# Kernel optimization log

Hardware: AMD Instinct MI355X
Metric: run time of the kernel (lower is better)

## Reference

```python
import jax, jax.numpy as jnp
import numpy as np

B, T, D = 4, 2048, 2048
DI = int(D * 2.0)  # mlp_expansion = 2.0
RMS_EPS = 1e-6
LRU_EPS = 1e-6
INIT_SCALE = 0.02


def _rmsnorm(x, w):
    return x * jax.lax.rsqrt(jnp.mean(x * x, axis=-1, keepdims=True) + RMS_EPS) * w


def setup_inputs() -> dict:
    key = jax.random.key(0)
    ks = jax.random.split(key, 10)
    s = INIT_SCALE
    return {
        "x": jax.random.normal(ks[0], (B, T, D), dtype=jnp.float32),
        "state": jnp.zeros((B, D), dtype=jnp.float32),
        "w_norm1": jnp.ones((D,), dtype=jnp.float32),
        "W_in": jax.random.normal(ks[1], (D, D), dtype=jnp.float32) * s,
        "W_r": jax.random.normal(ks[2], (D, D), dtype=jnp.float32) * s,
        "b_r": jnp.zeros((D,), dtype=jnp.float32),
        "W_i": jax.random.normal(ks[3], (D, D), dtype=jnp.float32) * s,
        "b_i": jnp.zeros((D,), dtype=jnp.float32),
        "log_decay": jax.random.normal(ks[4], (D,), dtype=jnp.float32),
        "W_out": jax.random.normal(ks[5], (D, D), dtype=jnp.float32) * s,
        "w_norm2": jnp.ones((D,), dtype=jnp.float32),
        "W_gate": jax.random.normal(ks[6], (DI, D), dtype=jnp.float32) * s,
        "W_up": jax.random.normal(ks[7], (DI, D), dtype=jnp.float32) * s,
        "W_down": jax.random.normal(ks[8], (D, DI), dtype=jnp.float32) * s,
    }


def reference(x, state, w_norm1, W_in, W_r, b_r, W_i, b_i, log_decay,
              W_out, w_norm2, W_gate, W_up, W_down):
    # --- pre-norm + RG-LRU mixer ---
    n = _rmsnorm(x, w_norm1)                      # (B,T,D)
    r = jax.nn.sigmoid(n @ W_r.T + b_r)           # input gate
    g = jax.nn.sigmoid(n @ W_i.T + b_i)           # recurrent gate
    xp = n @ W_in.T                               # projected input
    alpha = jnp.clip(jax.nn.sigmoid(log_decay), LRU_EPS, 1.0 - LRU_EPS)  # (D,)
    scale = jnp.sqrt(jnp.clip(1.0 - alpha * alpha, 0.0, None))           # (D,)
    b_seq = scale * (r * xp)                      # (B,T,D)

    def step(h, b_t):                             # h_t = alpha*h + scale*(r_t*x_t)
        h = alpha * h + b_t
        return h, h

    h_final, hs = jax.lax.scan(step, state, jnp.swapaxes(b_seq, 0, 1))  # hs: (T,B,D)
    hs = jnp.swapaxes(hs, 0, 1)                   # (B,T,D)
    mixer_out = (hs * g) @ W_out.T
    x = x + mixer_out

    # --- SwiGLU FFN ---
    n2 = _rmsnorm(x, w_norm2)
    ffn = (jax.nn.silu(n2 @ W_gate.T) * (n2 @ W_up.T)) @ W_down.T
    return x + ffn, h_final
```

## Files before the change

### kernel.cpp

```cpp
#include <hip/hip_runtime.h>

#define BD 4
#define TD 2048
#define DD 2048
#define DID 4096
#define MD (BD*TD)
#define CHK 32
#define CHL (TD/CHK)

typedef float f32x4 __attribute__((ext_vector_type(4)));
typedef short s16x8 __attribute__((ext_vector_type(8)));
typedef unsigned short u16;
typedef unsigned short u16x4 __attribute__((ext_vector_type(4)));
typedef unsigned short u16x8 __attribute__((ext_vector_type(8)));

__device__ __forceinline__ float bf2f(u16 u) {
    union { unsigned int i; float f; } v; v.i = ((unsigned int)u) << 16; return v.f;
}
__device__ __forceinline__ u16 f2bf(float f) {
    union { float f; unsigned int i; } v; v.f = f;
    unsigned int r = v.i + 0x7fffu + ((v.i >> 16) & 1u);
    return (u16)(r >> 16);
}
__device__ __forceinline__ float sigm(float x) { return 1.f / (1.f + __expf(-x)); }

__device__ __forceinline__ void mfma16(f32x4& acc, s16x8 a, s16x8 b) {
    asm("v_mfma_f32_16x16x32_bf16 %0, %1, %2, %0" : "+v"(acc) : "v"(a), "v"(b));
}

__device__ __forceinline__ void gload16(const u16* g, u16* l) {
    __builtin_amdgcn_global_load_lds((__attribute__((address_space(1))) void*)(g),
                                     (__attribute__((address_space(3))) void*)(l),
                                     16, 0, 0);
}

__global__ __launch_bounds__(256)
void cvt_all(const float4* __restrict__ sr, const float4* __restrict__ sin_,
             const float4* __restrict__ si, const float4* __restrict__ sout,
             const float4* __restrict__ sg, const float4* __restrict__ su,
             const float4* __restrict__ sd, u16x4* __restrict__ dst, int n4) {
    const int SEG  = DD * DD / 4;
    const int ROWQ = DD / 4;
    int i = blockIdx.x * blockDim.x + threadIdx.x;
    int stride = gridDim.x * blockDim.x;
    for (; i < n4; i += stride) {
        const float4* s; int off; size_t di;
        if (i < 2 * SEG) {
            int which = i / SEG;
            int jj = i - which * SEG;
            int g = jj / ROWQ, cq = jj - g * ROWQ;
            int nb = g >> 6, ii = g & 63;
            int dr = which == 0 ? nb * 128 + (ii < 32 ? ii : ii + 32)
                                : nb * 128 + (ii < 32 ? ii + 32 : ii + 64);
            s = which ? sin_ : sr; off = jj;
            di = (size_t)dr * ROWQ + cq;
        } else if (i < 3 * SEG) {
            s = si; off = i - 2 * SEG; di = i;
        } else if (i < 4 * SEG) {
            s = sout; off = i - 3 * SEG; di = i;
        } else if (i < 8 * SEG) {
            int j = i - 4 * SEG;
            int which = j / (2 * SEG);
            int jj = j - which * 2 * SEG;
            int g = jj / ROWQ, cq = jj - g * ROWQ;
            int nb = g >> 6, ii = g & 63;
            int dr = which == 0 ? nb * 128 + (ii < 32 ? ii : ii + 32)
                                : nb * 128 + (ii < 32 ? ii + 32 : ii + 64);
            s = which ? su : sg; off = jj;
            di = (size_t)4 * SEG + (size_t)dr * ROWQ + cq;
        } else {
            s = sd; off = i - 8 * SEG; di = i;
        }
        float4 v = s[off];
        u16x4 o = { f2bf(v.x), f2bf(v.y), f2bf(v.z), f2bf(v.w) };
        dst[di] = o;
    }
}

__global__ __launch_bounds__(256) void rmsnorm_kernel(const float* __restrict__ x,
                                                      const float* __restrict__ w,
                                                      u16* __restrict__ out) {
    const int row = blockIdx.x;
    const int tid = threadIdx.x;
    const float4* x4 = (const float4*)(x + (size_t)row * DD);
    float4 a = x4[tid * 2], b = x4[tid * 2 + 1];
    float s = a.x*a.x + a.y*a.y + a.z*a.z + a.w*a.w
            + b.x*b.x + b.y*b.y + b.z*b.z + b.w*b.w;
#pragma unroll
    for (int off = 32; off >= 1; off >>= 1) s += __shfl_xor(s, off, 64);
    __shared__ float red[4];
    if ((tid & 63) == 0) red[tid >> 6] = s;
    __syncthreads();
    float tot = red[0] + red[1] + red[2] + red[3];
    float rs = rsqrtf(tot * (1.f / DD) + 1e-6f);
    const float4* w4 = (const float4*)w;
    float4 wa = w4[tid * 2], wb = w4[tid * 2 + 1];
    u16x8 o = { f2bf(a.x*rs*wa.x), f2bf(a.y*rs*wa.y), f2bf(a.z*rs*wa.z), f2bf(a.w*rs*wa.w),
                f2bf(b.x*rs*wb.x), f2bf(b.y*rs*wb.y), f2bf(b.z*rs*wb.z), f2bf(b.w*rs*wb.w) };
    *(u16x8*)(out + (size_t)row * DD + tid * 8) = o;
}

template<int EPI>
__global__ __launch_bounds__(256)
void gemm_bt(const u16* __restrict__ A, const u16* __restrict__ Bw,
             int M, int N, int K,
             const float* __restrict__ bias0,
             const float* resid, float* outf,
             u16* __restrict__ out0, int Dsub) {
    __shared__ __align__(16) u16 lA[128 * 64];
    __shared__ __align__(16) u16 lB[128 * 64];
    const int tid  = threadIdx.x;
    const int lane = tid & 63;
    const int wave = tid >> 6;
    const int wr = (wave >> 1) << 6;
    const int wc = (wave & 1) << 6;
    const int brow = blockIdx.x * 128;
    const int bcol = blockIdx.y * 128;

    const int srow  = tid >> 3;
    const int schnk = (tid & 7) ^ (srow & 7);
    const size_t soff = (size_t)srow * K + (schnk << 3);
    const u16* gA = A  + (size_t)brow * K + soff;
    const u16* gB = Bw + (size_t)bcol * K + soff;
    u16* lAp = lA + tid * 8;
    u16* lBp = lB + tid * 8;

    const int fr = lane & 15;
    const int lg = lane >> 4;
    const int ck0 = ((lg)     ^ (fr & 7)) << 4;
    const int ck1 = ((4 + lg) ^ (fr & 7)) << 4;
    const char* lAc = (const char*)lA;
    const char* lBc = (const char*)lB;

    f32x4 acc[4][4];
#pragma unroll
    for (int i = 0; i < 4; ++i)
#pragma unroll
        for (int j = 0; j < 4; ++j)
            acc[i][j] = (f32x4){0.f, 0.f, 0.f, 0.f};

    for (int k0 = 0; k0 < K; k0 += 64) {
#pragma unroll
        for (int s = 0; s < 4; ++s) {
            gload16(gA + k0 + (size_t)s * 32 * K, lAp + s * 2048);
            gload16(gB + k0 + (size_t)s * 32 * K, lBp + s * 2048);
        }
        __syncthreads();
        s16x8 af[4][2], bq[4][2];
#pragma unroll
        for (int i = 0; i < 4; ++i) {
            const int ra = (wr + i * 16 + fr) * 128;
            const int rb = (wc + i * 16 + fr) * 128;
            af[i][0] = *(const s16x8*)(lAc + ra + ck0);
            af[i][1] = *(const s16x8*)(lAc + ra + ck1);
            bq[i][0] = *(const s16x8*)(lBc + rb + ck0);
            bq[i][1] = *(const s16x8*)(lBc + rb + ck1);
        }
#pragma unroll
        for (int h = 0; h < 2; ++h)
#pragma unroll
            for (int i = 0; i < 4; ++i)
#pragma unroll
                for (int j = 0; j < 4; ++j)
                    mfma16(acc[i][j], af[i][h], bq[j][h]);
        __syncthreads();
    }

#pragma unroll
    for (int i = 0; i < 4; ++i)
#pragma unroll
        for (int j = 0; j < 4; ++j)
            asm volatile("s_nop 7" : "+v"(acc[i][j]));

    const int r0 = brow + wr + (lg << 2);

    if (EPI == 3 || EPI == 4) {
        const int nb = bcol >> 7;
        const int cbase = nb * 64 + (wc ? 32 : 0);
#pragma unroll
        for (int i = 0; i < 4; ++i)
#pragma unroll
            for (int j = 0; j < 2; ++j)
#pragma unroll
                for (int e = 0; e < 4; ++e) {
                    const int grow = r0 + i * 16 + e;
                    const int col  = cbase + j * 16 + fr;
                    const float g = acc[i][j][e];
                    const float u = acc[i][j + 2][e];
                    float v;
                    if (EPI == 3) v = g * sigm(g) * u;
                    else          v = sigm(g + bias0[col]) * u;
                    out0[(size_t)grow * Dsub + col] = f2bf(v);
                }
        return;
    }

    const int c0 = bcol + wc + fr;
#pragma unroll
    for (int i = 0; i < 4; ++i) {
#pragma unroll
        for (int j = 0; j < 4; ++j) {
            const int gcol = c0 + j * 16;
#pragma unroll
            for (int e = 0; e < 4; ++e) {
                const int grow = r0 + i * 16 + e;
                float c = acc[i][j][e];
                if (EPI == 1) {
                    const size_t idx = (size_t)grow * N + gcol;
                    outf[idx] = resid[idx] + c;
                } else {
                    out0[(size_t)grow * Dsub + gcol] = f2bf(sigm(c + bias0[gcol]));
                }
            }
        }
    }
}

__global__ __launch_bounds__(256)
void scan_partial(const u16* __restrict__ BP,
                  const float* __restrict__ log_dec, float* __restrict__ carry) {
    const int d = blockIdx.x * 256 + threadIdx.x;
    const int k = blockIdx.y;
    const int b = blockIdx.z;
    float a = sigm(log_dec[d]);
    a = fminf(fmaxf(a, 1e-6f), 1.f - 1e-6f);
    const float sc = sqrtf(fmaxf(1.f - a * a, 0.f));
    float h = 0.f;
    size_t idx = ((size_t)b * TD + (size_t)k * CHL) * DD + d;
#pragma unroll 8
    for (int t = 0; t < CHL; ++t) {
        h = a * h + sc * bf2f(BP[idx]);
        idx += DD;
    }
    carry[((size_t)b * CHK + k) * DD + d] = h;
}

__global__ __launch_bounds__(256)
void scan_carry(const float* __restrict__ state, const float* __restrict__ log_dec,
                const float* __restrict__ carry, float* __restrict__ carryin,
                float* __restrict__ hfin) {
    const int d = blockIdx.x * 256 + threadIdx.x;
    const int b = blockIdx.y;
    float a = sigm(log_dec[d]);
    a = fminf(fmaxf(a, 1e-6f), 1.f - 1e-6f);
    float aL = a;
#pragma unroll
    for (int i = 0; i < 6; ++i) aL *= aL;
    float h = state[(size_t)b * DD + d];
#pragma unroll
    for (int k = 0; k < CHK; ++k) {
        const size_t ci = ((size_t)b * CHK + k) * DD + d;
        carryin[ci] = h;
        h = aL * h + carry[ci];
    }
    hfin[(size_t)b * DD + d] = h;
}

__global__ __launch_bounds__(256)
void scan_final(const u16* __restrict__ BP, const u16* __restrict__ G,
                const float* __restrict__ log_dec,
                const float* __restrict__ carryin, u16* __restrict__ HSG) {
    const int d = blockIdx.x * 256 + threadIdx.x;
    const int k = blockIdx.y;
    const int b = blockIdx.z;
    float a = sigm(log_dec[d]);
    a = fminf(fmaxf(a, 1e-6f), 1.f - 1e-6f);
    const float sc = sqrtf(fmaxf(1.f - a * a, 0.f));
    float h = carryin[((size_t)b * CHK + k) * DD + d];
    size_t idx = ((size_t)b * TD + (size_t)k * CHL) * DD + d;
#pragma unroll 8
    for (int t = 0; t < CHL; ++t) {
        h = a * h + sc * bf2f(BP[idx]);
        HSG[idx] = f2bf(h * bf2f(G[idx]));
        idx += DD;
    }
}

extern "C" void kernel_launch(void* const* d_in, const int* in_sizes, int n_in,
                              void* d_out, int out_size, void* d_ws, size_t ws_size,
                              hipStream_t stream) {
    const float* x       = (const float*)d_in[0];
    const float* state   = (const float*)d_in[1];
    const float* w_norm1 = (const float*)d_in[2];
    const float* W_in    = (const float*)d_in[3];
    const float* W_r     = (const float*)d_in[4];
    const float* b_r     = (const float*)d_in[5];
    const float* W_i     = (const float*)d_in[6];
    const float* b_i     = (const float*)d_in[7];
    const float* log_dec = (const float*)d_in[8];
    const float* W_out   = (const float*)d_in[9];
    const float* w_norm2 = (const float*)d_in[10];
    const float* W_gate  = (const float*)d_in[11];
    const float* W_up    = (const float*)d_in[12];
    const float* W_down  = (const float*)d_in[13];

    float* out  = (float*)d_out;
    float* hfin = out + (size_t)MD * DD;

    const size_t SEGU = (size_t)DD * DD;
    u16* w_rx    = (u16*)d_ws;
    u16* w_i     = w_rx   + 2 * SEGU;
    u16* w_out   = w_rx   + 3 * SEGU;
    u16* w_gu    = w_rx   + 4 * SEGU;
    u16* w_down  = w_rx   + 8 * SEGU;
    u16* bufN    = w_rx   + 10 * SEGU;
    u16* bufBP   = bufN   + (size_t)MD * DD;
    u16* bufG    = bufBP  + (size_t)MD * DD;
    u16* spare   = bufG   + (size_t)MD * DD;
    float* carry   = (float*)spare;
    float* carryin = carry + (size_t)BD * CHK * DD;

    cvt_all<<<2048, 256, 0, stream>>>((const float4*)W_r, (const float4*)W_in,
                                      (const float4*)W_i, (const float4*)W_out,
                                      (const float4*)W_gate, (const float4*)W_up,
                                      (const float4*)W_down, (u16x4*)w_rx,
                                      (int)(10 * SEGU / 4));

    rmsnorm_kernel<<<MD, 256, 0, stream>>>(x, w_norm1, bufN);

    {
        dim3 g1(MD / 128, (2 * DD) / 128);
        gemm_bt<4><<<g1, 256, 0, stream>>>(bufN, w_rx, MD, 2 * DD, DD,
                                           b_r, nullptr, nullptr, bufBP, DD);
    }
    {
        dim3 g1b(MD / 128, DD / 128);
        gemm_bt<5><<<g1b, 256, 0, stream>>>(bufN, w_i, MD, DD, DD,
                                            b_i, nullptr, nullptr, bufG, DD);
    }

    {
        dim3 gp(DD / 256, CHK, BD);
        scan_partial<<<gp, 256, 0, stream>>>(bufBP, log_dec, carry);
        dim3 gc(DD / 256, BD);
        scan_carry<<<gc, 256, 0, stream>>>(state, log_dec, carry, carryin, hfin);
        scan_final<<<gp, 256, 0, stream>>>(bufBP, bufG, log_dec, carryin, bufN);
    }

    {
        dim3 g2(MD / 128, DD / 128);
        gemm_bt<1><<<g2, 256, 0, stream>>>(bufN, w_out, MD, DD, DD,
                                           nullptr, x, out, nullptr, 0);
    }

    rmsnorm_kernel<<<MD, 256, 0, stream>>>(out, w_norm2, bufN);

    {
        dim3 g3(MD / 128, (2 * DID) / 128);
        gemm_bt<3><<<g3, 256, 0, stream>>>(bufN, w_gu, MD, 2 * DID, DD,
                                           nullptr, nullptr, nullptr, bufBP, DID);
    }

    {
        dim3 g4(MD / 128, DD / 128);
        gemm_bt<1><<<g4, 256, 0, stream>>>(bufBP, w_down, MD, DD, DID,
                                           nullptr, out, out, nullptr, 0);
    }
}
```

Before: 816.7 us.

## Fuse W_i gate GEMM into r/x GEMM and merge scan carry pass into final

Combines the recurrent-gate projection with the input-gate/projection GEMM into a single launch whose epilogue branches on column range to write either the gated input or the sigmoid gate. The three-kernel chunked scan becomes two: each final-pass block recomputes its incoming carry by serially folding the preceding chunk carries, and the last chunk writes h_final. Scan kernels are vectorised to four channels per thread. This removes two launches and a carry buffer round trip, at the cost of redundant serial carry work in later chunks and fewer scan threads.

Measured after the change: 819.5 us. No clear change (+0.3%).

```diff
diff --git a/kernel.cpp b/kernel.cpp
--- a/kernel.cpp
+++ b/kernel.cpp
@@ -104,9 +104,9 @@
 __global__ __launch_bounds__(256)
 void gemm_bt(const u16* __restrict__ A, const u16* __restrict__ Bw,
              int M, int N, int K,
-             const float* __restrict__ bias0,
+             const float* __restrict__ bias0, const float* __restrict__ bias1,
              const float* resid, float* outf,
-             u16* __restrict__ out0, int Dsub) {
+             u16* __restrict__ out0, u16* __restrict__ out1, int Dsub) {
     __shared__ __align__(16) u16 lA[128 * 64];
     __shared__ __align__(16) u16 lB[128 * 64];
     const int tid  = threadIdx.x;
@@ -174,7 +174,7 @@
 
     const int r0 = brow + wr + (lg << 2);
 
-    if (EPI == 3 || EPI == 4) {
+    if (EPI == 3 || (EPI == 6 && bcol < 2 * DD)) {
         const int nb = bcol >> 7;
         const int cbase = nb * 64 + (wc ? 32 : 0);
 #pragma unroll
@@ -209,7 +209,8 @@
                     const size_t idx = (size_t)grow * N + gcol;
                     outf[idx] = resid[idx] + c;
                 } else {
-                    out0[(size_t)grow * Dsub + gcol] = f2bf(sigm(c + bias0[gcol]));
+                    const int gc = gcol - 2 * DD;
+                    out1[(size_t)grow * Dsub + gc] = f2bf(sigm(c + bias1[gc]));
                 }
             }
         }
@@ -217,62 +218,75 @@
 }
 
 __global__ __launch_bounds__(256)
-void scan_partial(const u16* __restrict__ BP,
-                  const float* __restrict__ log_dec, float* __restrict__ carry) {
-    const int d = blockIdx.x * 256 + threadIdx.x;
+void scan_partial(const u16x4* __restrict__ BP4,
+                  const float4* __restrict__ ld4, float4* __restrict__ carry4) {
+    const int d4 = blockIdx.x * 256 + threadIdx.x;
     const int k = blockIdx.y;
     const int b = blockIdx.z;
-    float a = sigm(log_dec[d]);
-    a = fminf(fmaxf(a, 1e-6f), 1.f - 1e-6f);
-    const float sc = sqrtf(fmaxf(1.f - a * a, 0.f));
-    float h = 0.f;
-    size_t idx = ((size_t)b * TD + (size_t)k * CHL) * DD + d;
+    const float4 ld = ld4[d4];
+    float a[4], sc[4], h[4];
+#pragma unroll
+    for (int c = 0; c < 4; ++c) {
+        float av = sigm(((const float*)&ld)[c]);
+        av = fminf(fmaxf(av, 1e-6f), 1.f - 1e-6f);
+        a[c] = av; sc[c] = sqrtf(fmaxf(1.f - av * av, 0.f)); h[c] = 0.f;
+    }
+    size_t idx = (((size_t)b * TD + (size_t)k * CHL) * DD >> 2) + d4;
 #pragma unroll 8
     for (int t = 0; t < CHL; ++t) {
-        h = a * h + sc * bf2f(BP[idx]);
-        idx += DD;
-    }
-    carry[((size_t)b * CHK + k) * DD + d] = h;
+        u16x4 bp = BP4[idx];
+#pragma unroll
+        for (int c = 0; c < 4; ++c) h[c] = a[c] * h[c] + sc[c] * bf2f(bp[c]);
+        idx += DD >> 2;
+    }
+    float4 o = { h[0], h[1], h[2], h[3] };
+    carry4[(((size_t)b * CHK + k) * DD >> 2) + d4] = o;
 }
 
 __global__ __launch_bounds__(256)
-void scan_carry(const float* __restrict__ state, const float* __restrict__ log_dec,
-                const float* __restrict__ carry, float* __restrict__ carryin,
-                float* __restrict__ hfin) {
-    const int d = blockIdx.x * 256 + threadIdx.x;
-    const int b = blockIdx.y;
-    float a = sigm(log_dec[d]);
-    a = fminf(fmaxf(a, 1e-6f), 1.f - 1e-6f);
-    float aL = a;
-#pragma unroll
-    for (int i = 0; i < 6; ++i) aL *= aL;
-    float h = state[(size_t)b * DD + d];
-#pragma unroll
-    for (int k = 0; k < CHK; ++k) {
-        const size_t ci = ((size_t)b * CHK + k) * DD + d;
-        carryin[ci] = h;
-        h = aL * h + carry[ci];
-    }
-    hfin[(size_t)b * DD + d] = h;
-}
-
-__global__ __launch_bounds__(256)
-void scan_final(const u16* __restrict__ BP, const u16* __restrict__ G,
-                const float* __restrict__ log_dec,
-                const float* __restrict__ carryin, u16* __restrict__ HSG) {
-    const int d = blockIdx.x * 256 + threadIdx.x;
+void scan_final(const u16x4* __restrict__ BP4, const u16x4* __restrict__ G4,
+                const float4* __restrict__ ld4, const float4* __restrict__ state4,
+                const float4* __restrict__ carry4,
+                u16x4* __restrict__ HSG4, float4* __restrict__ hfin4) {
+    const int d4 = blockIdx.x * 256 + threadIdx.x;
     const int k = blockIdx.y;
     const int b = blockIdx.z;
-    float a = sigm(log_dec[d]);
-    a = fminf(fmaxf(a, 1e-6f), 1.f - 1e-6f);
-    const float sc = sqrtf(fmaxf(1.f - a * a, 0.f));
-    float h = carryin[((size_t)b * CHK + k) * DD + d];
-    size_t idx = ((size_t)b * TD + (size_t)k * CHL) * DD + d;
+    const float4 ld = ld4[d4];
+    float a[4], sc[4], aL[4], h[4];
+    const float4 st = state4[((size_t)b * DD >> 2) + d4];
+#pragma unroll
+    for (int c = 0; c < 4; ++c) {
+        float av = sigm(((const float*)&ld)[c]);
+        av = fminf(fmaxf(av, 1e-6f), 1.f - 1e-6f);
+        a[c] = av; sc[c] = sqrtf(fmaxf(1.f - av * av, 0.f));
+        float p = av;
+#pragma unroll
+        for (int i = 0; i < 6; ++i) p *= p;
+        aL[c] = p;
+        h[c] = ((const float*)&st)[c];
+    }
+    for (int kk = 0; kk < k; ++kk) {
+        float4 cv = carry4[(((size_t)b * CHK + kk) * DD >> 2) + d4];
+#pragma unroll
+        for (int c = 0; c < 4; ++c) h[c] = aL[c] * h[c] + ((const float*)&cv)[c];
+    }
+    size_t idx = (((size_t)b * TD + (size_t)k * CHL) * DD >> 2) + d4;
 #pragma unroll 8
     for (int t = 0; t < CHL; ++t) {
-        h = a * h + sc * bf2f(BP[idx]);
-        HSG[idx] = f2bf(h * bf2f(G[idx]));
-        idx += DD;
+        u16x4 bp = BP4[idx];
+        u16x4 gv = G4[idx];
+        u16x4 o;
+#pragma unroll
+        for (int c = 0; c < 4; ++c) {
+            h[c] = a[c] * h[c] + sc[c] * bf2f(bp[c]);
+            o[c] = f2bf(h[c] * bf2f(gv[c]));
+        }
+        HSG4[idx] = o;
+        idx += DD >> 2;
+    }
+    if (k == CHK - 1) {
+        float4 o = { h[0], h[1], h[2], h[3] };
+        hfin4[((size_t)b * DD >> 2) + d4] = o;
     }
 }
 
@@ -299,7 +313,6 @@
 
     const size_t SEGU = (size_t)DD * DD;
     u16* w_rx    = (u16*)d_ws;
-    u16* w_i     = w_rx   + 2 * SEGU;
     u16* w_out   = w_rx   + 3 * SEGU;
     u16* w_gu    = w_rx   + 4 * SEGU;
     u16* w_down  = w_rx   + 8 * SEGU;
@@ -307,8 +320,7 @@
     u16* bufBP   = bufN   + (size_t)MD * DD;
     u16* bufG    = bufBP  + (size_t)MD * DD;
     u16* spare   = bufG   + (size_t)MD * DD;
-    float* carry   = (float*)spare;
-    float* carryin = carry + (size_t)BD * CHK * DD;
+    float* carry = (float*)spare;
 
     cvt_all<<<2048, 256, 0, stream>>>((const float4*)W_r, (const float4*)W_in,
                                       (const float4*)W_i, (const float4*)W_out,
@@ -319,28 +331,25 @@
     rmsnorm_kernel<<<MD, 256, 0, stream>>>(x, w_norm1, bufN);
 
     {
-        dim3 g1(MD / 128, (2 * DD) / 128);
-        gemm_bt<4><<<g1, 256, 0, stream>>>(bufN, w_rx, MD, 2 * DD, DD,
-                                           b_r, nullptr, nullptr, bufBP, DD);
-    }
-    {
-        dim3 g1b(MD / 128, DD / 128);
-        gemm_bt<5><<<g1b, 256, 0, stream>>>(bufN, w_i, MD, DD, DD,
-                                            b_i, nullptr, nullptr, bufG, DD);
-    }
-
-    {
-        dim3 gp(DD / 256, CHK, BD);
-        scan_partial<<<gp, 256, 0, stream>>>(bufBP, log_dec, carry);
-        dim3 gc(DD / 256, BD);
-        scan_carry<<<gc, 256, 0, stream>>>(state, log_dec, carry, carryin, hfin);
-        scan_final<<<gp, 256, 0, stream>>>(bufBP, bufG, log_dec, carryin, bufN);
+        dim3 g1(MD / 128, (3 * DD) / 128);
+        gemm_bt<6><<<g1, 256, 0, stream>>>(bufN, w_rx, MD, 3 * DD, DD,
+                                           b_r, b_i, nullptr, nullptr, bufBP, bufG, DD);
+    }
+
+    {
+        dim3 gp(DD / 1024, CHK, BD);
+        scan_partial<<<gp, 256, 0, stream>>>((const u16x4*)bufBP,
+                                             (const float4*)log_dec, (float4*)carry);
+        scan_final<<<gp, 256, 0, stream>>>((const u16x4*)bufBP, (const u16x4*)bufG,
+                                           (const float4*)log_dec, (const float4*)state,
+                                           (const float4*)carry,
+                                           (u16x4*)bufN, (float4*)hfin);
     }
 
     {
         dim3 g2(MD / 128, DD / 128);
         gemm_bt<1><<<g2, 256, 0, stream>>>(bufN, w_out, MD, DD, DD,
-                                           nullptr, x, out, nullptr, 0);
+                                           nullptr, nullptr, x, out, nullptr, nullptr, 0);
     }
 
     rmsnorm_kernel<<<MD, 256, 0, stream>>>(out, w_norm2, bufN);
@@ -348,12 +357,12 @@
     {
         dim3 g3(MD / 128, (2 * DID) / 128);
         gemm_bt<3><<<g3, 256, 0, stream>>>(bufN, w_gu, MD, 2 * DID, DD,
-                                           nullptr, nullptr, nullptr, bufBP, DID);
+                                           nullptr, nullptr, nullptr, nullptr, bufBP, nullptr, DID);
     }
 
     {
         dim3 g4(MD / 128, DD / 128);
         gemm_bt<1><<<g4, 256, 0, stream>>>(bufBP, w_down, MD, DD, DID,
-                                           nullptr, out, out, nullptr, 0);
-    }
-}
+                                           nullptr, nullptr, out, out, nullptr, nullptr, 0);
+    }
+}
```
